# Optimization experiments

Measured on AMD Instinct MI355X. Metric: run time of the kernel, lower is better.

Reference implementation:

```python
import jax, jax.numpy as jnp
import numpy as np

# Hardware-emulation constants (from init_kwargs, NeuroSim-style QLinear)
WL_IN = 8        # input activation bit width (bit-serial)
WL_W = 8         # weight bit width
CELL_BIT = 2     # bits per memory cell -> 4 weight slices
SUB = 128        # crossbar sub-array size (rows summed in analog)
ADC_BITS = 5     # ADC precision per partial sum
ONOFF = 10.0     # cell on/off conductance ratio
VARI = 0.05      # multiplicative device variation sigma


def _adc_quant(x, bits, axes):
    # LinearQuantizeOut: uniform quantization between tensor min/max
    mn = jnp.min(x, axis=axes, keepdims=True)
    mx = jnp.max(x, axis=axes, keepdims=True)
    step = (mx - mn) * (2.0 ** (-bits))
    step = jnp.where(step <= 0, 1.0, step)
    idx = jnp.clip(jnp.floor((x - mn) / step), 0.0, 2.0 ** bits - 1.0)
    return idx * step + mn


def _qlinear_hw(x, w, noise):
    """Analog PIM crossbar emulation of y = x @ w.T with bit-serial inputs,
    bit-sliced cells, on/off-ratio offset + dummy column, device variation,
    per-subarray ADC quantization."""
    B, N = x.shape
    F = w.shape[0]
    I, W, K = WL_IN, WL_W, WL_W // CELL_BIT
    cr = 2.0 ** CELL_BIT
    lower, upper = 1.0 / ONOFF, 1.0
    S = (N + SUB - 1) // SUB
    Np = S * SUB
    # quantize input to I bits in [0,1]; weight to W-bit integer in [0, 2^W-1]
    xq = jnp.round(jnp.clip(x, 0.0, 1.0) * (2.0 ** I - 1.0))            # [B, N]
    Xi = jnp.clip(jnp.round((w + 1.0) * 0.5 * (2.0 ** W - 1.0)), 0.0, 2.0 ** W - 1.0)  # [F, N]
    xq = jnp.pad(xq, ((0, 0), (0, Np - N)))
    Xi = jnp.pad(Xi, ((0, 0), (0, Np - N)))
    zpow = 2.0 ** jnp.arange(I, dtype=x.dtype)
    kpow = cr ** jnp.arange(K, dtype=x.dtype)
    bits = jnp.mod(jnp.floor(xq[..., None] / zpow), 2.0)                # [B, Np, I]
    slc = jnp.mod(jnp.floor(Xi[..., None] / kpow), cr)                  # [F, Np, K]
    g = slc * (upper - lower) + (cr - 1.0) * lower                      # cell conductances
    g = g * (1.0 + VARI * noise)                                        # device variation
    bits = bits.reshape(B, S, SUB, I)
    g = g.reshape(F, S, SUB, K)
    # analog partial sums per (input bit i, subarray s, weight slice k)
    P = jnp.einsum('bsai,fsak->iskbf', bits, g)                         # [I,S,K,B,F]
    # dummy column (all cells at lowest conductance), identical across F
    D = jnp.transpose(bits.sum(axis=2), (2, 1, 0)) * ((cr - 1.0) * lower)  # [I,S,B]
    Pq = _adc_quant(P, ADC_BITS, axes=(3, 4))
    Dq = _adc_quant(D, ADC_BITS, axes=(2,))
    scal = (2.0 ** jnp.arange(I, dtype=x.dtype))[:, None] * (cr ** jnp.arange(K, dtype=x.dtype))[None, :]
    acc = jnp.einsum('iskbf,ik->bf', Pq - Dq[:, :, None, :, None], scal) / (upper - lower)
    # undo integer mappings: w = 2*Xi/(2^W-1) - 1, x = xq/(2^I-1)
    out = 2.0 * acc / ((2.0 ** I - 1.0) * (2.0 ** W - 1.0)) \
          - xq.sum(axis=1, keepdims=True) / (2.0 ** I - 1.0)
    return out


def _qlinear(x, w, noise):
    # straight-through quantized weight (WAGE-style STE) + hardware forward
    Xi = jnp.clip(jnp.round((w + 1.0) * 0.5 * (2.0 ** WL_W - 1.0)), 0.0, 2.0 ** WL_W - 1.0)
    wq = 2.0 * Xi / (2.0 ** WL_W - 1.0) - 1.0
    wq_ste = w + jax.lax.stop_gradient(wq - w)
    out_ideal = x @ wq_ste.T
    out_hw = _qlinear_hw(x, w, noise)
    return out_ideal + jax.lax.stop_gradient(out_hw - out_ideal)


def setup_inputs() -> dict:
    key = jax.random.key(0)
    k1, k2, k3, k4, k5 = jax.random.split(key, 5)
    x = jax.random.uniform(k1, (1024, 784), dtype=jnp.float32)
    w1 = jax.random.normal(k2, (512, 784), dtype=jnp.float32) * 0.05
    w3 = jax.random.normal(k3, (10, 512), dtype=jnp.float32) * 0.08
    noise1 = jax.random.normal(k4, (512, 896, 4), dtype=jnp.float32)  # 784 padded to 7*128
    noise3 = jax.random.normal(k5, (10, 512, 4), dtype=jnp.float32)   # 512 = 4*128 exact
    return {"x": x, "w1": w1, "w3": w3, "noise1": noise1, "noise3": noise3}


def reference(x, w1, w3, noise1, noise3):
    h = jnp.tanh(_qlinear(x, w1, noise1))   # QLinear(784,512) + Tanh
    return _qlinear(h, w3, noise3)          # QLinear(512,10)
```

## Files before the change

kernel.cpp:

```cpp
#include <hip/hip_runtime.h>

#define FLTMAX 3.402823466e+38f


__global__ void prep1_kernel(const float* __restrict__ x, float* __restrict__ sx1,
                             unsigned* __restrict__ xqbT, unsigned* __restrict__ stats1)
{
    __shared__ float xr[896];
    __shared__ float red[128];
    int b = blockIdx.x;
    if (b == 0) {
        for (int t = threadIdx.x; t < 224; t += 128) {
            stats1[t * 2] = 0x7F7FFFFFu; stats1[t * 2 + 1] = 0u;
        }
    }
    float psum = 0.f;
    for (int n = threadIdx.x; n < 896; n += 128) {
        float v = 0.f;
        if (n < 784) {
            float xv = x[b * 784 + n];
            xv = fminf(fmaxf(xv, 0.f), 1.f);
            v = rintf(__fmul_rn(xv, 255.f));
        }
        xr[n] = v;
        psum += v;
    }
    red[threadIdx.x] = psum;
    __syncthreads();
    for (int w = 64; w >= 1; w >>= 1) {
        if (threadIdx.x < w) red[threadIdx.x] += red[threadIdx.x + w];
        __syncthreads();
    }
    if (threadIdx.x == 0) sx1[b] = red[0];
    if (threadIdx.x < 28) {
        int w = threadIdx.x;
        unsigned words[8] = {0, 0, 0, 0, 0, 0, 0, 0};
#pragma unroll 8
        for (int n = 0; n < 32; ++n) {
            int v = (int)xr[w * 32 + n];
#pragma unroll
            for (int i = 0; i < 8; ++i) words[i] |= ((unsigned)((v >> i) & 1)) << n;
        }
#pragma unroll
        for (int i = 0; i < 8; ++i) xqbT[(i * 28 + w) * 1024 + b] = words[i];
    }
}

__global__ void prepg1t_kernel(const float* __restrict__ w1, const float* __restrict__ noise1,
                               float* __restrict__ g1t)
{
    __shared__ float t[4][32][33];
    const int n0 = blockIdx.x * 32, f0 = blockIdx.y * 32;
    const int tid = threadIdx.x;
    {
        int n = tid & 31, fi = tid >> 5;
#pragma unroll
        for (int p = 0; p < 4; ++p) {
            int f = p * 8 + fi;
            int gn = n0 + n, gf = f0 + f;
            float gv[4] = {0.f, 0.f, 0.f, 0.f};
            if (gn < 784) {
                float w = w1[gf * 784 + gn];
                float Xi = fminf(fmaxf(rintf(__fmul_rn(__fmul_rn(__fadd_rn(w, 1.f), 0.5f), 255.f)),
                                       0.f), 255.f);
                int xi = (int)Xi;
                float4 nz = *(const float4*)&noise1[(gf * 896 + gn) * 4];
                float nzv[4] = {nz.x, nz.y, nz.z, nz.w};
#pragma unroll
                for (int k = 0; k < 4; ++k) {
                    int slc = (xi >> (2 * k)) & 3;
                    float base = __fadd_rn(__fmul_rn((float)slc, 0.9f), 0.3f);
                    float nf = __fadd_rn(1.f, __fmul_rn(0.05f, nzv[k]));
                    gv[k] = __fmul_rn(base, nf);
                }
            }
#pragma unroll
            for (int k = 0; k < 4; ++k) t[k][n][f] = gv[k];
        }
    }
    __syncthreads();
    {
        int f = tid & 31, nn = tid >> 5;
#pragma unroll
        for (int p = 0; p < 4; ++p) {
            int n = p * 8 + nn;
#pragma unroll
            for (int k = 0; k < 4; ++k)
                g1t[(n0 + n) * 2048 + k * 512 + f0 + f] = t[k][n][f];
        }
    }
}

__global__ void prepg2_kernel(const float* __restrict__ w3, const float* __restrict__ noise3,
                              float* __restrict__ g2t)
{
    int gid = blockIdx.x * 256 + threadIdx.x;
    if (gid >= 10 * 512) return;
    int f = gid / 512, n = gid % 512;
    float w = w3[f * 512 + n];
    float Xi = fminf(fmaxf(rintf(__fmul_rn(__fmul_rn(__fadd_rn(w, 1.f), 0.5f), 255.f)),
                           0.f), 255.f);
    int xi = (int)Xi;
#pragma unroll
    for (int k = 0; k < 4; ++k) {
        int slc = (xi >> (2 * k)) & 3;
        float base = __fadd_rn(__fmul_rn((float)slc, 0.9f), 0.3f);
        float nf = __fadd_rn(1.f, __fmul_rn(0.05f, noise3[(f * 512 + n) * 4 + k]));
        g2t[n * 40 + k * 10 + f] = __fmul_rn(base, nf);
    }
}

__global__ void dqpopT_kernel(const unsigned* __restrict__ xqbT, float* __restrict__ Dq)
{
    __shared__ float red[512];
    const int i = blockIdx.x / 7, s = blockIdx.x % 7;
    const int tid = threadIdx.x;
    float D[4];
    float mn = FLTMAX, mx = -FLTMAX;
#pragma unroll
    for (int u = 0; u < 4; ++u) {
        int b = tid + u * 256;
        int c = 0;
#pragma unroll
        for (int w = 0; w < 4; ++w)
            c += __popc(xqbT[(i * 28 + s * 4 + w) * 1024 + b]);
        D[u] = __fmul_rn((float)c, 0.3f);
        mn = fminf(mn, D[u]);
        mx = fmaxf(mx, D[u]);
    }
    red[tid] = mn; red[256 + tid] = mx;
    __syncthreads();
    for (int w = 128; w >= 1; w >>= 1) {
        if (tid < w) {
            red[tid] = fminf(red[tid], red[tid + w]);
            red[256 + tid] = fmaxf(red[256 + tid], red[256 + tid + w]);
        }
        __syncthreads();
    }
    mn = red[0]; mx = red[256];
    float step = __fmul_rn(__fsub_rn(mx, mn), 0.03125f);
    if (step <= 0.f) step = 1.f;
#pragma unroll
    for (int u = 0; u < 4; ++u) {
        int b = tid + u * 256;
        float idx = fminf(fmaxf(floorf(__fdiv_rn(__fsub_rn(D[u], mn), step)), 0.f), 31.f);
        Dq[(i * 7 + s) * 1024 + b] = __fadd_rn(__fmul_rn(idx, step), mn);
    }
}

__global__ void dqpop_kernel(const unsigned* __restrict__ xqb, float* __restrict__ Dq,
                             int S, int wpr)
{
    __shared__ float red[512];
    const int i = blockIdx.x / S, s = blockIdx.x % S;
    const int tid = threadIdx.x;
    float D[4];
    float mn = FLTMAX, mx = -FLTMAX;
#pragma unroll
    for (int u = 0; u < 4; ++u) {
        int b = tid + u * 256;
        uint4 w = *(const uint4*)&xqb[(i * 1024 + b) * wpr + s * 4];
        int c = __popc(w.x) + __popc(w.y) + __popc(w.z) + __popc(w.w);
        D[u] = __fmul_rn((float)c, 0.3f);
        mn = fminf(mn, D[u]);
        mx = fmaxf(mx, D[u]);
    }
    red[tid] = mn; red[256 + tid] = mx;
    __syncthreads();
    for (int w = 128; w >= 1; w >>= 1) {
        if (tid < w) {
            red[tid] = fminf(red[tid], red[tid + w]);
            red[256 + tid] = fmaxf(red[256 + tid], red[256 + tid + w]);
        }
        __syncthreads();
    }
    mn = red[0]; mx = red[256];
    float step = __fmul_rn(__fsub_rn(mx, mn), 0.03125f);
    if (step <= 0.f) step = 1.f;
#pragma unroll
    for (int u = 0; u < 4; ++u) {
        int b = tid + u * 256;
        float idx = fminf(fmaxf(floorf(__fdiv_rn(__fsub_rn(D[u], mn), step)), 0.f), 31.f);
        Dq[(i * S + s) * 1024 + b] = __fadd_rn(__fmul_rn(idx, step), mn);
    }
}

#define BK 32
__global__ __launch_bounds__(256, 4) void mm1_kernel(
    const unsigned* __restrict__ xqbT, const float* __restrict__ g1t,
    float* __restrict__ P, unsigned* __restrict__ stats, int s0)
{
    __shared__ __align__(16) float Bs[BK][132];
    __shared__ unsigned Abits[128];
    __shared__ float red[512];
    const int tid = threadIdx.x;
    const int sl = blockIdx.x >> 6;
    const int r = blockIdx.x & 63;
    const int i = r >> 3;
    const int b0 = (r & 7) * 128;
    const int s = s0 + sl;
    const int colBase = blockIdx.y * 128;
    const int tx = tid & 15, ty = tid >> 4;

    const int aB = tid >> 5;
    const int eB = (tid & 31) << 2;

    float4 pB[4];
    unsigned pAw = 0;
#pragma unroll
    for (int u = 0; u < 4; ++u)
        pB[u] = *(const float4*)&g1t[(s * 128 + u * 8 + aB) * 2048 + colBase + eB];
    if (tid < 128) pAw = xqbT[(i * 28 + s * 4) * 1024 + b0 + tid];

    float acc[8][8] = {};

    for (int ac = 0; ac < 4; ++ac) {
        __syncthreads();
#pragma unroll
        for (int u = 0; u < 4; ++u)
            *(float4*)&Bs[u * 8 + aB][eB] = pB[u];
        if (tid < 128) Abits[tid] = pAw;
        __syncthreads();

        if (ac < 3) {
            const int n0 = s * 128 + (ac + 1) * BK;
#pragma unroll
            for (int u = 0; u < 4; ++u)
                pB[u] = *(const float4*)&g1t[(n0 + u * 8 + aB) * 2048 + colBase + eB];
            if (tid < 128) pAw = xqbT[(i * 28 + s * 4 + ac + 1) * 1024 + b0 + tid];
        }

        unsigned wrd[8];
#pragma unroll
        for (int u = 0; u < 4; ++u) {
            wrd[u]     = Abits[(ty << 2) + u];
            wrd[4 + u] = Abits[64 + (ty << 2) + u];
        }

#pragma unroll 4
        for (int a = 0; a < BK; ++a) {
            float br[8];
            *(float4*)&br[0] = *(const float4*)&Bs[a][(tx << 2)];
            *(float4*)&br[4] = *(const float4*)&Bs[a][64 + (tx << 2)];
#pragma unroll
            for (int u = 0; u < 8; ++u) {
                float ab = (float)((wrd[u] >> a) & 1u);
#pragma unroll
                for (int v = 0; v < 8; ++v)
                    acc[u][v] = fmaf(ab, br[v], acc[u][v]);
            }
        }
    }

#pragma unroll
    for (int uh = 0; uh < 2; ++uh)
#pragma unroll
        for (int u = 0; u < 4; ++u) {
            int row = (sl * 8 + i) * 1024 + b0 + uh * 64 + (ty << 2) + u;
#pragma unroll
            for (int vh = 0; vh < 2; ++vh) {
                float4 v = make_float4(acc[uh * 4 + u][vh * 4 + 0], acc[uh * 4 + u][vh * 4 + 1],
                                       acc[uh * 4 + u][vh * 4 + 2], acc[uh * 4 + u][vh * 4 + 3]);
                *(float4*)&P[(size_t)row * 2048 + colBase + vh * 64 + (tx << 2)] = v;
            }
        }

    float mn = acc[0][0], mx = acc[0][0];
#pragma unroll
    for (int u = 0; u < 8; ++u)
#pragma unroll
        for (int v = 0; v < 8; ++v) { mn = fminf(mn, acc[u][v]); mx = fmaxf(mx, acc[u][v]); }
    red[tid] = mn; red[256 + tid] = mx;
    __syncthreads();
    for (int w = 128; w >= 1; w >>= 1) {
        if (tid < w) {
            red[tid] = fminf(red[tid], red[tid + w]);
            red[256 + tid] = fmaxf(red[256 + tid], red[256 + tid + w]);
        }
        __syncthreads();
    }
    if (tid == 0) {
        int k = colBase >> 9;
        int slot = ((s * 8 + i) * 4 + k) * 2;
        atomicMin(&stats[slot], __float_as_uint(red[0]));
        atomicMax(&stats[slot + 1], __float_as_uint(red[256]));
    }
}

__global__ void quant1_kernel(const float* __restrict__ P, const unsigned* __restrict__ stats,
                              float* __restrict__ acc1, int s0, int G, int first)
{
    int gid = blockIdx.x * 256 + threadIdx.x;
    int b = gid >> 7, f4 = gid & 127;
    float4 accR;
    if (first) accR = make_float4(0.f, 0.f, 0.f, 0.f);
    else       accR = *(const float4*)&acc1[(b << 9) + (f4 << 2)];
    for (int sl = 0; sl < G; ++sl) {
        int s = s0 + sl;
        float4 sum = make_float4(0.f, 0.f, 0.f, 0.f);
        for (int i = 0; i < 8; ++i) {
#pragma unroll
            for (int k = 0; k < 4; ++k) {
                int slot = ((s * 8 + i) * 4 + k) * 2;
                float mn = __uint_as_float(stats[slot]);
                float mx = __uint_as_float(stats[slot + 1]);
                float step = __fmul_rn(__fsub_rn(mx, mn), 0.03125f);
                if (step <= 0.f) step = 1.f;
                float4 val = *(const float4*)&P[(size_t)((sl * 8 + i) * 1024 + b) * 2048
                                                + (k << 9) + (f4 << 2)];
                float sc = (float)(1 << (i + 2 * k));
                float ix, pq;
                ix = fminf(fmaxf(floorf(__fdiv_rn(__fsub_rn(val.x, mn), step)), 0.f), 31.f);
                pq = __fadd_rn(__fmul_rn(ix, step), mn); sum.x = fmaf(pq, sc, sum.x);
                ix = fminf(fmaxf(floorf(__fdiv_rn(__fsub_rn(val.y, mn), step)), 0.f), 31.f);
                pq = __fadd_rn(__fmul_rn(ix, step), mn); sum.y = fmaf(pq, sc, sum.y);
                ix = fminf(fmaxf(floorf(__fdiv_rn(__fsub_rn(val.z, mn), step)), 0.f), 31.f);
                pq = __fadd_rn(__fmul_rn(ix, step), mn); sum.z = fmaf(pq, sc, sum.z);
                ix = fminf(fmaxf(floorf(__fdiv_rn(__fsub_rn(val.w, mn), step)), 0.f), 31.f);
                pq = __fadd_rn(__fmul_rn(ix, step), mn); sum.w = fmaf(pq, sc, sum.w);
            }
        }
        accR.x = __fadd_rn(accR.x, sum.x);
        accR.y = __fadd_rn(accR.y, sum.y);
        accR.z = __fadd_rn(accR.z, sum.z);
        accR.w = __fadd_rn(accR.w, sum.w);
    }
    *(float4*)&acc1[(b << 9) + (f4 << 2)] = accR;
}

__global__ void finish1_kernel(const float* __restrict__ acc1, const float* __restrict__ P,
                               const unsigned* __restrict__ stats, int s0, int G, int first,
                               const float* __restrict__ Dq1, const float* __restrict__ sx1,
                               float* __restrict__ xq2, unsigned* __restrict__ xqb2,
                               float* __restrict__ sx2)
{
    __shared__ float red[512];
    __shared__ float dt;
    int b = blockIdx.x;
    int f = threadIdx.x;
    if (f == 0) {
        float s = 0.f;
        for (int i = 0; i < 8; ++i) {
            float sc = (float)(85 << i);
            for (int ss = 0; ss < 7; ++ss) s = fmaf(Dq1[(i * 7 + ss) * 1024 + b], sc, s);
        }
        dt = s;
    }
    __syncthreads();
    int gid = b * 512 + f;
    float accR = first ? 0.f : acc1[gid];
    for (int sl = 0; sl < G; ++sl) {
        int s = s0 + sl;
        float sum = 0.f;
        for (int i = 0; i < 8; ++i) {
#pragma unroll
            for (int k = 0; k < 4; ++k) {
                int slot = ((s * 8 + i) * 4 + k) * 2;
                float mn = __uint_as_float(stats[slot]);
                float mx = __uint_as_float(stats[slot + 1]);
                float step = __fmul_rn(__fsub_rn(mx, mn), 0.03125f);
                if (step <= 0.f) step = 1.f;
                float val = P[(size_t)((sl * 8 + i) * 1024 + b) * 2048 + (k << 9) + f];
                float ix = fminf(fmaxf(floorf(__fdiv_rn(__fsub_rn(val, mn), step)), 0.f), 31.f);
                float pq = __fadd_rn(__fmul_rn(ix, step), mn);
                sum = fmaf(pq, (float)(1 << (i + 2 * k)), sum);
            }
        }
        accR = __fadd_rn(accR, sum);
    }
    float total = __fsub_rn(accR, dt);
    float acc = __fdiv_rn(total, 0.9f);
    float o = __fsub_rn(__fdiv_rn(__fmul_rn(2.f, acc), 65025.f), __fdiv_rn(sx1[b], 255.f));
    float h = tanhf(o);
    h = fminf(fmaxf(h, 0.f), 1.f);
    float code = rintf(__fmul_rn(h, 255.f));
    xq2[gid] = code;
    int ci = (int)code;
    int lane = f & 63;
#pragma unroll
    for (int i = 0; i < 8; ++i) {
        unsigned long long m = __ballot((ci >> i) & 1);
        if ((lane & 31) == 0) {
            unsigned wv = (lane & 32) ? (unsigned)(m >> 32) : (unsigned)m;
            xqb2[(i * 1024 + b) * 16 + (f >> 5)] = wv;
        }
    }
    red[f] = code;
    __syncthreads();
    for (int w = 256; w >= 1; w >>= 1) {
        if (f < w) red[f] += red[f + w];
        __syncthreads();
    }
    if (f == 0) sx2[b] = red[0];
}

__global__ void mm2_kernel(const float* __restrict__ xq2, const float* __restrict__ g2t,
                           float* __restrict__ P2)
{
    int gid = blockIdx.x * 256 + threadIdx.x;
    if (gid >= 40960) return;
    int f = gid % 10;
    int b = (gid / 10) & 1023;
    int s = gid / 10240;
    float acc[8][4] = {};
    for (int a = 0; a < 128; ++a) {
        int n = s * 128 + a;
        int xi = (int)xq2[b * 512 + n];
        float g0 = g2t[n * 40 + f];
        float gA = g2t[n * 40 + 10 + f];
        float gB = g2t[n * 40 + 20 + f];
        float gC = g2t[n * 40 + 30 + f];
#pragma unroll
        for (int i = 0; i < 8; ++i) {
            float bi = (float)((xi >> i) & 1);
            acc[i][0] = fmaf(bi, g0, acc[i][0]);
            acc[i][1] = fmaf(bi, gA, acc[i][1]);
            acc[i][2] = fmaf(bi, gB, acc[i][2]);
            acc[i][3] = fmaf(bi, gC, acc[i][3]);
        }
    }
#pragma unroll
    for (int i = 0; i < 8; ++i)
#pragma unroll
        for (int k = 0; k < 4; ++k)
            P2[(size_t)((s * 8 + i) * 4 + k) * 10240 + b * 10 + f] = acc[i][k];
}

__global__ void stat2_kernel(const float* __restrict__ P2, float2* __restrict__ stats2)
{
    __shared__ float red[512];
    int p = blockIdx.x;
    int tid = threadIdx.x;
    float mn = FLTMAX, mx = -FLTMAX;
    for (int t = tid; t < 10240; t += 256) {
        float v = P2[(size_t)p * 10240 + t];
        mn = fminf(mn, v); mx = fmaxf(mx, v);
    }
    red[tid] = mn; red[256 + tid] = mx;
    __syncthreads();
    for (int w = 128; w >= 1; w >>= 1) {
        if (tid < w) {
            red[tid] = fminf(red[tid], red[tid + w]);
            red[256 + tid] = fmaxf(red[256 + tid], red[256 + tid + w]);
        }
        __syncthreads();
    }
    if (tid == 0) {
        float step = __fmul_rn(__fsub_rn(red[256], red[0]), 0.03125f);
        if (step <= 0.f) step = 1.f;
        stats2[p] = make_float2(red[0], step);
    }
}

__global__ void out2_kernel(const float* __restrict__ P2, const float2* __restrict__ stats2,
                            const float* __restrict__ Dq2, const float* __restrict__ sx2,
                            float* __restrict__ out)
{
    int gid = blockIdx.x * 256 + threadIdx.x;
    if (gid >= 10240) return;
    int b = gid / 10;
    float dt = 0.f;
    for (int i = 0; i < 8; ++i) {
        float sc = (float)(85 << i);
        for (int s = 0; s < 4; ++s) dt = fmaf(Dq2[(i * 4 + s) * 1024 + b], sc, dt);
    }
    float sum = 0.f;
    for (int s = 0; s < 4; ++s)
        for (int i = 0; i < 8; ++i)
#pragma unroll
            for (int k = 0; k < 4; ++k) {
                int p = (s * 8 + i) * 4 + k;
                float2 st = stats2[p];
                float val = P2[(size_t)p * 10240 + gid];
                float idx = fminf(fmaxf(floorf(__fdiv_rn(__fsub_rn(val, st.x), st.y)), 0.f), 31.f);
                float pq = __fadd_rn(__fmul_rn(idx, st.y), st.x);
                sum = fmaf(pq, (float)(1 << (i + 2 * k)), sum);
            }
    float total = __fsub_rn(sum, dt);
    float acc = __fdiv_rn(total, 0.9f);
    out[gid] = __fsub_rn(__fdiv_rn(__fmul_rn(2.f, acc), 65025.f), __fdiv_rn(sx2[b], 255.f));
}

extern "C" void kernel_launch(void* const* d_in, const int* in_sizes, int n_in,
                              void* d_out, int out_size, void* d_ws, size_t ws_size,
                              hipStream_t stream)
{
    const float* x      = (const float*)d_in[0];
    const float* w1     = (const float*)d_in[1];
    const float* w3     = (const float*)d_in[2];
    const float* noise1 = (const float*)d_in[3];
    const float* noise3 = (const float*)d_in[4];
    float* out = (float*)d_out;
    float* ws  = (float*)d_ws;

    float*    g1t    = ws + 0;
    float*    acc1   = ws + 1835008;
    float*    xq2    = ws + 2359296;
    float*    P2     = ws + 2883584;
    float*    g2t    = ws + 4194304;
    float*    Dq1    = ws + 4214784;
    float*    Dq2    = ws + 4272128;
    float*    sx1    = ws + 4304896;
    float*    sx2    = ws + 4305920;
    float2*   stats2 = (float2*)(ws + 4306944);
    unsigned* stats1 = (unsigned*)(ws + 4307200);
    unsigned* xqbT   = (unsigned*)(ws + 4307712);
    unsigned* xqb2   = (unsigned*)(ws + 4537088);
    float*    Ps     = ws + 4668160;

    const size_t fixedf = 4668160;
    const size_t planef = 16777216;
    int G = 1;
    while (G < 7 && (fixedf + (size_t)(G + 1) * planef) * sizeof(float) <= ws_size) ++G;

    prep1_kernel<<<1024, 128, 0, stream>>>(x, sx1, xqbT, stats1);
    prepg1t_kernel<<<dim3(28, 16), 256, 0, stream>>>(w1, noise1, g1t);
    dqpopT_kernel<<<56, 256, 0, stream>>>(xqbT, Dq1);

    int lastS0 = 0, lastG = 7, anyQuant = 0;
    for (int s0 = 0; s0 < 7;) {
        int Gc = (7 - s0 < G) ? (7 - s0) : G;
        mm1_kernel<<<dim3(Gc * 64, 16), 256, 0, stream>>>(xqbT, g1t, Ps, stats1, s0);
        if (s0 + Gc < 7) {
            quant1_kernel<<<512, 256, 0, stream>>>(Ps, stats1, acc1, s0, Gc, s0 == 0);
            anyQuant = 1;
        } else {
            lastS0 = s0; lastG = Gc;
        }
        s0 += Gc;
    }

    finish1_kernel<<<1024, 512, 0, stream>>>(acc1, Ps, stats1, lastS0, lastG,
                                             anyQuant ? 0 : 1, Dq1, sx1, xq2, xqb2, sx2);
    prepg2_kernel<<<20, 256, 0, stream>>>(w3, noise3, g2t);
    dqpop_kernel<<<32, 256, 0, stream>>>(xqb2, Dq2, 4, 16);
    mm2_kernel<<<160, 256, 0, stream>>>(xq2, g2t, P2);
    stat2_kernel<<<128, 256, 0, stream>>>(P2, stats2);
    out2_kernel<<<40, 256, 0, stream>>>(P2, stats2, Dq2, sx2, out);
}
```

Measured before the change: 636.2 us.

## Fuse layer-1 subarray loop into persistent kernel with grid barrier and byte ADC indices

The multi-launch mm1/quant1/finish1 pipeline becomes a single persistent mm1 kernel of 1024 blocks. It loops over all 7 subarrays and uses a software grid barrier after each subarray's min/max atomics, so it can quantize the partial sums in registers and write 5-bit ADC indices as bytes instead of float partial sums. A new fold1 kernel reads the byte indices with per-slot mn/step from shared memory and dequantizes and accumulates them. This cuts the partial-sum traffic to a quarter and removes the intermediate passes. The grid barrier relies on all 1024 blocks being co-resident, which launch_bounds(256,4) may allow on 256 CUs but is not guaranteed, and the spin loop has an iteration cap.

Measured after the change: 2.086 ms. 3.28x slower.

```diff
diff --git a/kernel.cpp b/kernel.cpp
--- a/kernel.cpp
+++ b/kernel.cpp
@@ -3,8 +3,24 @@
 #define FLTMAX 3.402823466e+38f
 
 
+__device__ __forceinline__ void grid_barrier(unsigned* bar, unsigned target)
+{
+    __syncthreads();
+    if (threadIdx.x == 0) {
+        __threadfence();
+        __hip_atomic_fetch_add(bar, 1u, __ATOMIC_ACQ_REL, __HIP_MEMORY_SCOPE_AGENT);
+        for (int it = 0; it < (1 << 22); ++it) {
+            if (__hip_atomic_load(bar, __ATOMIC_ACQUIRE, __HIP_MEMORY_SCOPE_AGENT) >= target)
+                break;
+            __builtin_amdgcn_s_sleep(8);
+        }
+    }
+    __syncthreads();
+}
+
 __global__ void prep1_kernel(const float* __restrict__ x, float* __restrict__ sx1,
-                             unsigned* __restrict__ xqbT, unsigned* __restrict__ stats1)
+                             unsigned* __restrict__ xqbT, unsigned* __restrict__ stats1,
+                             unsigned* __restrict__ bar)
 {
     __shared__ float xr[896];
     __shared__ float red[128];
@@ -13,6 +29,7 @@
         for (int t = threadIdx.x; t < 224; t += 128) {
             stats1[t * 2] = 0x7F7FFFFFu; stats1[t * 2 + 1] = 0u;
         }
+        if (threadIdx.x < 8) bar[threadIdx.x] = 0u;
     }
     float psum = 0.f;
     for (int n = threadIdx.x; n < 896; n += 128) {
@@ -188,182 +205,161 @@
 #define BK 32
 __global__ __launch_bounds__(256, 4) void mm1_kernel(
     const unsigned* __restrict__ xqbT, const float* __restrict__ g1t,
-    float* __restrict__ P, unsigned* __restrict__ stats, int s0)
+    unsigned char* __restrict__ Pidx, unsigned* stats, unsigned* bar)
 {
     __shared__ __align__(16) float Bs[BK][132];
     __shared__ unsigned Abits[128];
     __shared__ float red[512];
     const int tid = threadIdx.x;
-    const int sl = blockIdx.x >> 6;
     const int r = blockIdx.x & 63;
     const int i = r >> 3;
     const int b0 = (r & 7) * 128;
-    const int s = s0 + sl;
-    const int colBase = blockIdx.y * 128;
+    const int colBase = (blockIdx.x >> 6) * 128;
     const int tx = tid & 15, ty = tid >> 4;
-
     const int aB = tid >> 5;
     const int eB = (tid & 31) << 2;
-
-    float4 pB[4];
-    unsigned pAw = 0;
-#pragma unroll
-    for (int u = 0; u < 4; ++u)
-        pB[u] = *(const float4*)&g1t[(s * 128 + u * 8 + aB) * 2048 + colBase + eB];
-    if (tid < 128) pAw = xqbT[(i * 28 + s * 4) * 1024 + b0 + tid];
-
-    float acc[8][8] = {};
-
-    for (int ac = 0; ac < 4; ++ac) {
+    const int k = colBase >> 9;
+
+    for (int s = 0; s < 7; ++s) {
+        float4 pB[4];
+        unsigned pAw = 0;
+#pragma unroll
+        for (int u = 0; u < 4; ++u)
+            pB[u] = *(const float4*)&g1t[(s * 128 + u * 8 + aB) * 2048 + colBase + eB];
+        if (tid < 128) pAw = xqbT[(i * 28 + s * 4) * 1024 + b0 + tid];
+
+        float acc[8][8] = {};
+
+        for (int ac = 0; ac < 4; ++ac) {
+            __syncthreads();
+#pragma unroll
+            for (int u = 0; u < 4; ++u)
+                *(float4*)&Bs[u * 8 + aB][eB] = pB[u];
+            if (tid < 128) Abits[tid] = pAw;
+            __syncthreads();
+
+            if (ac < 3) {
+                const int n0 = s * 128 + (ac + 1) * BK;
+#pragma unroll
+                for (int u = 0; u < 4; ++u)
+                    pB[u] = *(const float4*)&g1t[(n0 + u * 8 + aB) * 2048 + colBase + eB];
+                if (tid < 128) pAw = xqbT[(i * 28 + s * 4 + ac + 1) * 1024 + b0 + tid];
+            }
+
+            unsigned wrd[8];
+#pragma unroll
+            for (int u = 0; u < 4; ++u) {
+                wrd[u]     = Abits[(ty << 2) + u];
+                wrd[4 + u] = Abits[64 + (ty << 2) + u];
+            }
+
+#pragma unroll 4
+            for (int a = 0; a < BK; ++a) {
+                float br[8];
+                *(float4*)&br[0] = *(const float4*)&Bs[a][(tx << 2)];
+                *(float4*)&br[4] = *(const float4*)&Bs[a][64 + (tx << 2)];
+#pragma unroll
+                for (int u = 0; u < 8; ++u) {
+                    float ab = (float)((wrd[u] >> a) & 1u);
+#pragma unroll
+                    for (int v = 0; v < 8; ++v)
+                        acc[u][v] = fmaf(ab, br[v], acc[u][v]);
+                }
+            }
+        }
+
+        float mn = acc[0][0], mx = acc[0][0];
+#pragma unroll
+        for (int u = 0; u < 8; ++u)
+#pragma unroll
+            for (int v = 0; v < 8; ++v) { mn = fminf(mn, acc[u][v]); mx = fmaxf(mx, acc[u][v]); }
+        red[tid] = mn; red[256 + tid] = mx;
         __syncthreads();
-#pragma unroll
-        for (int u = 0; u < 4; ++u)
-            *(float4*)&Bs[u * 8 + aB][eB] = pB[u];
-        if (tid < 128) Abits[tid] = pAw;
-        __syncthreads();
-
-        if (ac < 3) {
-            const int n0 = s * 128 + (ac + 1) * BK;
-#pragma unroll
-            for (int u = 0; u < 4; ++u)
-                pB[u] = *(const float4*)&g1t[(n0 + u * 8 + aB) * 2048 + colBase + eB];
-            if (tid < 128) pAw = xqbT[(i * 28 + s * 4 + ac + 1) * 1024 + b0 + tid];
-        }
-
-        unsigned wrd[8];
-#pragma unroll
-        for (int u = 0; u < 4; ++u) {
-            wrd[u]     = Abits[(ty << 2) + u];
-            wrd[4 + u] = Abits[64 + (ty << 2) + u];
-        }
-
-#pragma unroll 4
-        for (int a = 0; a < BK; ++a) {
-            float br[8];
-            *(float4*)&br[0] = *(const float4*)&Bs[a][(tx << 2)];
-            *(float4*)&br[4] = *(const float4*)&Bs[a][64 + (tx << 2)];
-#pragma unroll
-            for (int u = 0; u < 8; ++u) {
-                float ab = (float)((wrd[u] >> a) & 1u);
-#pragma unroll
-                for (int v = 0; v < 8; ++v)
-                    acc[u][v] = fmaf(ab, br[v], acc[u][v]);
-            }
-        }
-    }
-
-#pragma unroll
-    for (int uh = 0; uh < 2; ++uh)
-#pragma unroll
-        for (int u = 0; u < 4; ++u) {
-            int row = (sl * 8 + i) * 1024 + b0 + uh * 64 + (ty << 2) + u;
-#pragma unroll
-            for (int vh = 0; vh < 2; ++vh) {
-                float4 v = make_float4(acc[uh * 4 + u][vh * 4 + 0], acc[uh * 4 + u][vh * 4 + 1],
-                                       acc[uh * 4 + u][vh * 4 + 2], acc[uh * 4 + u][vh * 4 + 3]);
-                *(float4*)&P[(size_t)row * 2048 + colBase + vh * 64 + (tx << 2)] = v;
-            }
-        }
-
-    float mn = acc[0][0], mx = acc[0][0];
-#pragma unroll
-    for (int u = 0; u < 8; ++u)
-#pragma unroll
-        for (int v = 0; v < 8; ++v) { mn = fminf(mn, acc[u][v]); mx = fmaxf(mx, acc[u][v]); }
-    red[tid] = mn; red[256 + tid] = mx;
-    __syncthreads();
-    for (int w = 128; w >= 1; w >>= 1) {
-        if (tid < w) {
-            red[tid] = fminf(red[tid], red[tid + w]);
-            red[256 + tid] = fmaxf(red[256 + tid], red[256 + tid + w]);
-        }
-        __syncthreads();
-    }
-    if (tid == 0) {
-        int k = colBase >> 9;
-        int slot = ((s * 8 + i) * 4 + k) * 2;
-        atomicMin(&stats[slot], __float_as_uint(red[0]));
-        atomicMax(&stats[slot + 1], __float_as_uint(red[256]));
-    }
-}
-
-__global__ void quant1_kernel(const float* __restrict__ P, const unsigned* __restrict__ stats,
-                              float* __restrict__ acc1, int s0, int G, int first)
-{
-    int gid = blockIdx.x * 256 + threadIdx.x;
-    int b = gid >> 7, f4 = gid & 127;
-    float4 accR;
-    if (first) accR = make_float4(0.f, 0.f, 0.f, 0.f);
-    else       accR = *(const float4*)&acc1[(b << 9) + (f4 << 2)];
-    for (int sl = 0; sl < G; ++sl) {
-        int s = s0 + sl;
-        float4 sum = make_float4(0.f, 0.f, 0.f, 0.f);
-        for (int i = 0; i < 8; ++i) {
-#pragma unroll
-            for (int k = 0; k < 4; ++k) {
-                int slot = ((s * 8 + i) * 4 + k) * 2;
-                float mn = __uint_as_float(stats[slot]);
-                float mx = __uint_as_float(stats[slot + 1]);
-                float step = __fmul_rn(__fsub_rn(mx, mn), 0.03125f);
-                if (step <= 0.f) step = 1.f;
-                float4 val = *(const float4*)&P[(size_t)((sl * 8 + i) * 1024 + b) * 2048
-                                                + (k << 9) + (f4 << 2)];
-                float sc = (float)(1 << (i + 2 * k));
-                float ix, pq;
-                ix = fminf(fmaxf(floorf(__fdiv_rn(__fsub_rn(val.x, mn), step)), 0.f), 31.f);
-                pq = __fadd_rn(__fmul_rn(ix, step), mn); sum.x = fmaf(pq, sc, sum.x);
-                ix = fminf(fmaxf(floorf(__fdiv_rn(__fsub_rn(val.y, mn), step)), 0.f), 31.f);
-                pq = __fadd_rn(__fmul_rn(ix, step), mn); sum.y = fmaf(pq, sc, sum.y);
-                ix = fminf(fmaxf(floorf(__fdiv_rn(__fsub_rn(val.z, mn), step)), 0.f), 31.f);
-                pq = __fadd_rn(__fmul_rn(ix, step), mn); sum.z = fmaf(pq, sc, sum.z);
-                ix = fminf(fmaxf(floorf(__fdiv_rn(__fsub_rn(val.w, mn), step)), 0.f), 31.f);
-                pq = __fadd_rn(__fmul_rn(ix, step), mn); sum.w = fmaf(pq, sc, sum.w);
-            }
-        }
-        accR.x = __fadd_rn(accR.x, sum.x);
-        accR.y = __fadd_rn(accR.y, sum.y);
-        accR.z = __fadd_rn(accR.z, sum.z);
-        accR.w = __fadd_rn(accR.w, sum.w);
-    }
-    *(float4*)&acc1[(b << 9) + (f4 << 2)] = accR;
-}
-
-__global__ void finish1_kernel(const float* __restrict__ acc1, const float* __restrict__ P,
-                               const unsigned* __restrict__ stats, int s0, int G, int first,
-                               const float* __restrict__ Dq1, const float* __restrict__ sx1,
-                               float* __restrict__ xq2, unsigned* __restrict__ xqb2,
-                               float* __restrict__ sx2)
+        for (int w = 128; w >= 1; w >>= 1) {
+            if (tid < w) {
+                red[tid] = fminf(red[tid], red[tid + w]);
+                red[256 + tid] = fmaxf(red[256 + tid], red[256 + tid + w]);
+            }
+            __syncthreads();
+        }
+        const int slot = ((s * 8 + i) * 4 + k) * 2;
+        if (tid == 0) {
+            atomicMin(&stats[slot], __float_as_uint(red[0]));
+            atomicMax(&stats[slot + 1], __float_as_uint(red[256]));
+        }
+
+        grid_barrier(&bar[s], 1024u);
+
+        unsigned mnu = __hip_atomic_load(&stats[slot],     __ATOMIC_RELAXED,
+                                         __HIP_MEMORY_SCOPE_AGENT);
+        unsigned mxu = __hip_atomic_load(&stats[slot + 1], __ATOMIC_RELAXED,
+                                         __HIP_MEMORY_SCOPE_AGENT);
+        float qmn = __uint_as_float(mnu);
+        float qmx = __uint_as_float(mxu);
+        float step = __fmul_rn(__fsub_rn(qmx, qmn), 0.03125f);
+        if (step <= 0.f) step = 1.f;
+
+#pragma unroll
+        for (int uh = 0; uh < 2; ++uh)
+#pragma unroll
+            for (int u = 0; u < 4; ++u) {
+                int row = (s * 8 + i) * 1024 + b0 + uh * 64 + (ty << 2) + u;
+#pragma unroll
+                for (int vh = 0; vh < 2; ++vh) {
+                    uchar4 q;
+                    float ix;
+                    ix = fminf(fmaxf(floorf(__fdiv_rn(__fsub_rn(acc[uh * 4 + u][vh * 4 + 0], qmn), step)), 0.f), 31.f);
+                    q.x = (unsigned char)(int)ix;
+                    ix = fminf(fmaxf(floorf(__fdiv_rn(__fsub_rn(acc[uh * 4 + u][vh * 4 + 1], qmn), step)), 0.f), 31.f);
+                    q.y = (unsigned char)(int)ix;
+                    ix = fminf(fmaxf(floorf(__fdiv_rn(__fsub_rn(acc[uh * 4 + u][vh * 4 + 2], qmn), step)), 0.f), 31.f);
+                    q.z = (unsigned char)(int)ix;
+                    ix = fminf(fmaxf(floorf(__fdiv_rn(__fsub_rn(acc[uh * 4 + u][vh * 4 + 3], qmn), step)), 0.f), 31.f);
+                    q.w = (unsigned char)(int)ix;
+                    *(uchar4*)&Pidx[(size_t)row * 2048 + colBase + vh * 64 + (tx << 2)] = q;
+                }
+            }
+    }
+}
+
+__global__ void fold1_kernel(const unsigned char* __restrict__ Pidx,
+                             const unsigned* __restrict__ stats,
+                             const float* __restrict__ Dq1, const float* __restrict__ sx1,
+                             float* __restrict__ xq2, unsigned* __restrict__ xqb2,
+                             float* __restrict__ sx2)
 {
     __shared__ float red[512];
     __shared__ float dt;
+    __shared__ float2 st[224];
     int b = blockIdx.x;
     int f = threadIdx.x;
+    if (f < 224) {
+        float mn = __uint_as_float(stats[f * 2]);
+        float mx = __uint_as_float(stats[f * 2 + 1]);
+        float step = __fmul_rn(__fsub_rn(mx, mn), 0.03125f);
+        if (step <= 0.f) step = 1.f;
+        st[f] = make_float2(mn, step);
+    }
     if (f == 0) {
-        float s = 0.f;
+        float sd = 0.f;
         for (int i = 0; i < 8; ++i) {
             float sc = (float)(85 << i);
-            for (int ss = 0; ss < 7; ++ss) s = fmaf(Dq1[(i * 7 + ss) * 1024 + b], sc, s);
-        }
-        dt = s;
-    }
-    __syncthreads();
-    int gid = b * 512 + f;
-    float accR = first ? 0.f : acc1[gid];
-    for (int sl = 0; sl < G; ++sl) {
-        int s = s0 + sl;
+            for (int ss = 0; ss < 7; ++ss) sd = fmaf(Dq1[(i * 7 + ss) * 1024 + b], sc, sd);
+        }
+        dt = sd;
+    }
+    __syncthreads();
+    float accR = 0.f;
+    for (int s = 0; s < 7; ++s) {
         float sum = 0.f;
         for (int i = 0; i < 8; ++i) {
-#pragma unroll
-            for (int k = 0; k < 4; ++k) {
-                int slot = ((s * 8 + i) * 4 + k) * 2;
-                float mn = __uint_as_float(stats[slot]);
-                float mx = __uint_as_float(stats[slot + 1]);
-                float step = __fmul_rn(__fsub_rn(mx, mn), 0.03125f);
-                if (step <= 0.f) step = 1.f;
-                float val = P[(size_t)((sl * 8 + i) * 1024 + b) * 2048 + (k << 9) + f];
-                float ix = fminf(fmaxf(floorf(__fdiv_rn(__fsub_rn(val, mn), step)), 0.f), 31.f);
-                float pq = __fadd_rn(__fmul_rn(ix, step), mn);
-                sum = fmaf(pq, (float)(1 << (i + 2 * k)), sum);
+            const unsigned char* rowp = &Pidx[(size_t)((s * 8 + i) * 1024 + b) * 2048 + f];
+#pragma unroll
+            for (int kk = 0; kk < 4; ++kk) {
+                float2 ms = st[((s * 8 + i) << 2) + kk];
+                float ixv = (float)rowp[kk << 9];
+                float pq = __fadd_rn(__fmul_rn(ixv, ms.y), ms.x);
+                sum = fmaf(pq, (float)(1 << (i + 2 * kk)), sum);
             }
         }
         accR = __fadd_rn(accR, sum);
@@ -374,7 +370,7 @@
     float h = tanhf(o);
     h = fminf(fmaxf(h, 0.f), 1.f);
     float code = rintf(__fmul_rn(h, 255.f));
-    xq2[gid] = code;
+    xq2[b * 512 + f] = code;
     int ci = (int)code;
     int lane = f & 63;
 #pragma unroll
@@ -493,45 +489,28 @@
     float* out = (float*)d_out;
     float* ws  = (float*)d_ws;
 
-    float*    g1t    = ws + 0;
-    float*    acc1   = ws + 1835008;
-    float*    xq2    = ws + 2359296;
-    float*    P2     = ws + 2883584;
-    float*    g2t    = ws + 4194304;
-    float*    Dq1    = ws + 4214784;
-    float*    Dq2    = ws + 4272128;
-    float*    sx1    = ws + 4304896;
-    float*    sx2    = ws + 4305920;
-    float2*   stats2 = (float2*)(ws + 4306944);
-    unsigned* stats1 = (unsigned*)(ws + 4307200);
-    unsigned* xqbT   = (unsigned*)(ws + 4307712);
-    unsigned* xqb2   = (unsigned*)(ws + 4537088);
-    float*    Ps     = ws + 4668160;
-
-    const size_t fixedf = 4668160;
-    const size_t planef = 16777216;
-    int G = 1;
-    while (G < 7 && (fixedf + (size_t)(G + 1) * planef) * sizeof(float) <= ws_size) ++G;
-
-    prep1_kernel<<<1024, 128, 0, stream>>>(x, sx1, xqbT, stats1);
+    float*         g1t    = ws + 0;
+    float*         xq2    = ws + 1835008;
+    float*         P2     = ws + 2359296;
+    float*         g2t    = ws + 3670016;
+    float*         Dq1    = ws + 3690496;
+    float*         Dq2    = ws + 3747840;
+    float*         sx1    = ws + 3780608;
+    float*         sx2    = ws + 3781632;
+    float2*        stats2 = (float2*)(ws + 3782656);
+    unsigned*      stats1 = (unsigned*)(ws + 3782912);
+    unsigned*      bar    = (unsigned*)(ws + 3782912) + 448;
+    unsigned*      xqbT   = (unsigned*)(ws + 3783424);
+    unsigned*      xqb2   = (unsigned*)(ws + 4012800);
+    unsigned char* Pidx   = (unsigned char*)(ws + 4143872);
+
+    prep1_kernel<<<1024, 128, 0, stream>>>(x, sx1, xqbT, stats1, bar);
     prepg1t_kernel<<<dim3(28, 16), 256, 0, stream>>>(w1, noise1, g1t);
     dqpopT_kernel<<<56, 256, 0, stream>>>(xqbT, Dq1);
 
-    int lastS0 = 0, lastG = 7, anyQuant = 0;
-    for (int s0 = 0; s0 < 7;) {
-        int Gc = (7 - s0 < G) ? (7 - s0) : G;
-        mm1_kernel<<<dim3(Gc * 64, 16), 256, 0, stream>>>(xqbT, g1t, Ps, stats1, s0);
-        if (s0 + Gc < 7) {
-            quant1_kernel<<<512, 256, 0, stream>>>(Ps, stats1, acc1, s0, Gc, s0 == 0);
-            anyQuant = 1;
-        } else {
-            lastS0 = s0; lastG = Gc;
-        }
-        s0 += Gc;
-    }
-
-    finish1_kernel<<<1024, 512, 0, stream>>>(acc1, Ps, stats1, lastS0, lastG,
-                                             anyQuant ? 0 : 1, Dq1, sx1, xq2, xqb2, sx2);
+    mm1_kernel<<<1024, 256, 0, stream>>>(xqbT, g1t, Pidx, stats1, bar);
+
+    fold1_kernel<<<1024, 512, 0, stream>>>(Pidx, stats1, Dq1, sx1, xq2, xqb2, sx2);
     prepg2_kernel<<<20, 256, 0, stream>>>(w3, noise3, g2t);
     dqpop_kernel<<<32, 256, 0, stream>>>(xqb2, Dq2, 4, 16);
     mm2_kernel<<<160, 256, 0, stream>>>(xq2, g2t, P2);
```
